# Optimization experiments

Measured on AMD Instinct MI355X. Metric: run time of the kernel, lower is better.

## Reference

```python
import jax, jax.numpy as jnp
import numpy as np

B, H, N, C, E, D, L_OUT, LAYERS = 16, 64, 512, 3, 128, 32, 12, 2


def setup_inputs() -> dict:
    key = jax.random.key(0)
    ks = jax.random.split(key, 16)
    nrm = lambda k, s, sc=1.0: jax.random.normal(k, s, jnp.float32) * sc
    adj = jax.random.uniform(ks[0], (N, N), jnp.float32)
    adj = adj / adj.sum(axis=-1, keepdims=True)  # row-normalized prior adjacency
    return {
        "x_input": nrm(ks[1], (B, H, N, C)),
        "adj": adj,
        "Wf": nrm(ks[2], (3, E, 3 * C), 0.1),
        "Uf": nrm(ks[3], (3, E, E), 0.05),
        "bf": jnp.zeros((3, E), jnp.float32),
        "E1f": nrm(ks[4], (N, D)),
        "E2f": nrm(ks[5], (N, D)),
        "Wb": nrm(ks[6], (3, E, 3 * C), 0.1),
        "Ub": nrm(ks[7], (3, E, E), 0.05),
        "bb": jnp.zeros((3, E), jnp.float32),
        "E1b": nrm(ks[8], (N, D)),
        "E2b": nrm(ks[9], (N, D)),
        "dec_w": nrm(ks[10], (L_OUT, LAYERS, 2 * E), 0.05),  # Conv2d(layer_num->out_len, k=(1,2E)) squeezed
        "dec_b": jnp.zeros((L_OUT,), jnp.float32),
        "out_w": nrm(ks[11], (L_OUT, L_OUT), 0.1),  # 1x1 Conv2d squeezed
        "out_b": jnp.zeros((L_OUT,), jnp.float32),
    }


def _cell_step(c, xt, adj, A_dyn, W, U, b):
    # Graph-coupled GRU cell (IBNCell): xt [B,C,N], c [B,E,N].
    msg = jnp.concatenate(
        [xt,
         jnp.einsum('bcn,nm->bcm', xt, adj),      # prior-graph message passing
         jnp.einsum('bcn,nm->bcm', xt, A_dyn)],   # learned dynamic-graph message passing
        axis=1)  # [B, 3C, N]
    gx = jnp.einsum('goc,bcn->gbon', W, msg)  # 3 stacked gate projections
    r = jax.nn.sigmoid(gx[0] + jnp.einsum('oe,ben->bon', U[0], c) + b[0][:, None])
    u = jax.nn.sigmoid(gx[1] + jnp.einsum('oe,ben->bon', U[1], c) + b[1][:, None])
    g = jnp.tanh(gx[2] + jnp.einsum('oe,ben->bon', U[2], r * c) + b[2][:, None])
    return u * c + (1.0 - u) * g


def _forward(x_input, adj, Wf, Uf, bf, E1f, E2f, Wb, Ub, bb, E1b, E2b, dec_w, dec_b, out_w, out_b):
    # torch: x_input.transpose(-3,-1).transpose(-2,-1) -> [B,C,H,N]; scan layout [H,B,C,N]
    xs = jnp.transpose(x_input, (1, 0, 3, 2))
    A_f = jax.nn.softmax(jax.nn.relu(E1f @ E2f.T), axis=-1)  # dynamic adjacency, fwd cell
    A_b = jax.nn.softmax(jax.nn.relu(E1b @ E2b.T), axis=-1)  # dynamic adjacency, back cell
    c0 = jnp.zeros((xs.shape[1], Wf.shape[1], xs.shape[3]), xs.dtype)  # [B,E,N]

    def step_f(c, xt):
        cn = _cell_step(c, xt, adj, A_f, Wf, Uf, bf)
        return cn, None

    # Output only depends on the last timestep of the bidirectional concat:
    # forward branch -> final state after H steps; backward branch (after flip)
    # at t=H-1 -> its FIRST step (input x[H-1]). Dead per-step outputs elided.
    h_fwd, _ = jax.lax.scan(step_f, c0, xs)
    h_back0 = _cell_step(c0, xs[-1], adj, A_b, Wb, Ub, bb)
    last_ht = jnp.concatenate([h_fwd, h_back0], axis=1)  # [B, 2E, N]

    lt = jnp.transpose(last_ht, (0, 2, 1))  # [B, N, 2E]
    # layer loop z>0 is a no-op on current_layer_output -> final_result repeats last_ht
    final = jnp.broadcast_to(lt[:, None], (lt.shape[0], LAYERS, lt.shape[1], lt.shape[2]))
    h = jnp.einsum('blne,ole->bon', final, dec_w) + dec_b[:, None]  # decoder conv (1,2E)
    return jnp.einsum('oi,bin->bon', out_w, h) + out_b[:, None]  # 1x1 output conv -> [B,L_OUT,N]


def reference(x_input, adj, Wf, Uf, bf, E1f, E2f, Wb, Ub, bb, E1b, E2b, dec_w, dec_b, out_w, out_b):
    return _forward(x_input, adj, Wf, Uf, bf, E1f, E2f, Wb, Ub, bb, E1b, E2b, dec_w, dec_b, out_w, out_b)
```

## Files before the change

kernel.cpp:

```cpp
#include <hip/hip_runtime.h>


typedef _Float16 half8_t __attribute__((ext_vector_type(8)));
typedef __fp16 fp16x2_t __attribute__((ext_vector_type(2)));
typedef float float4_t __attribute__((ext_vector_type(4)));

#define PIN(x) asm volatile("" : "+v"(x))

__device__ __forceinline__ float exp2_(float x) { return __builtin_amdgcn_exp2f(x); }
__device__ __forceinline__ float rcp_(float x) { return __builtin_amdgcn_rcpf(x); }

__global__ __launch_bounds__(256) void prep_kernel(
    const float* __restrict__ E1f, const float* __restrict__ E2f,
    const float* __restrict__ E1b, const float* __restrict__ E2b,
    const float* __restrict__ adj, const float* __restrict__ Wf,
    const float* __restrict__ Uf, const float* __restrict__ bf,
    const float* __restrict__ Wb, const float* __restrict__ bb,
    _Float16* __restrict__ adjT, _Float16* __restrict__ AfT,
    _Float16* __restrict__ AbT, _Float16* __restrict__ ufrag,
    _Float16* __restrict__ wbfrag, _Float16* __restrict__ zpad) {
  int bid = blockIdx.x;
  int tid = threadIdx.x;
  if (bid >= 1288) {
    if (tid < 64) zpad[tid] = (_Float16)0.f;
    return;
  }
  if (bid >= 1272) {
    int r2 = bid - 1272;
    int gi = 1 + (r2 & 1);
    int og = r2 >> 1;
    float scl = (gi == 2) ? 2.8853902f : -1.4426950f;
    for (int e = tid; e < 512; e += 256) {
      int lane = e >> 3, j = e & 7;
      int o = og * 16 + (lane & 15);
      int q = (lane >> 4) * 8 + j;
      float v = (q < 9) ? Wb[gi * 1152 + o * 9 + q]
                        : (q == 9 ? bb[gi * 128 + o] : 0.f);
      wbfrag[r2 * 512 + e] = (_Float16)(v * scl);
    }
    return;
  }
  if (bid >= 1152) {
    int r = bid - 1152;
    int kb = r % 5;
    int gi = (r / 5) % 3;
    int og = r / 15;
    float scl = (gi == 2) ? 2.8853902f : -1.4426950f;
    for (int e = tid; e < 512; e += 256) {
      int lane = e >> 3, j = e & 7;
      int o = og * 16 + (lane & 15);
      int q4 = lane >> 4;
      float v;
      if (kb < 4) {
        v = Uf[gi * 16384 + o * 128 + kb * 32 + q4 * 8 + j];
      } else {
        int q = q4 * 8 + j;
        v = (q < 9) ? Wf[gi * 1152 + o * 9 + q]
                    : (q == 9 ? bf[gi * 128 + o] : 0.f);
      }
      ufrag[r * 512 + e] = (_Float16)(v * scl);
    }
    return;
  }
  if (bid >= 1024) {
    int base = (bid - 1024) * 4;
    for (int r = 0; r < 4; ++r) {
      int row = base + r;
      float v0 = adj[row * 512 + tid];
      float v1 = adj[row * 512 + tid + 256];
      adjT[(size_t)tid * 512 + row] = (_Float16)v0;
      adjT[(size_t)(tid + 256) * 512 + row] = (_Float16)v1;
    }
    return;
  }
  int which = bid >> 9;
  int row = bid & 511;
  const float* E1 = which ? E1b : E1f;
  const float* E2 = which ? E2b : E2f;
  _Float16* A = which ? AbT : AfT;
  __shared__ float e1s[32];
  __shared__ float red[256];
  if (tid < 32) e1s[tid] = E1[row * 32 + tid];
  __syncthreads();
  float s[2];
#pragma unroll
  for (int h = 0; h < 2; ++h) {
    int m = tid + h * 256;
    const float4* e2 = (const float4*)(E2 + m * 32);
    float acc = 0.f;
#pragma unroll
    for (int d4 = 0; d4 < 8; ++d4) {
      float4 v = e2[d4];
      acc = fmaf(v.x, e1s[d4 * 4 + 0], acc);
      acc = fmaf(v.y, e1s[d4 * 4 + 1], acc);
      acc = fmaf(v.z, e1s[d4 * 4 + 2], acc);
      acc = fmaf(v.w, e1s[d4 * 4 + 3], acc);
    }
    s[h] = fmaxf(acc, 0.f);
  }
  red[tid] = fmaxf(s[0], s[1]);
  __syncthreads();
  for (int off = 128; off > 0; off >>= 1) {
    if (tid < off) red[tid] = fmaxf(red[tid], red[tid + off]);
    __syncthreads();
  }
  float mx = red[0];
  __syncthreads();
  float e0 = __expf(s[0] - mx), e1v = __expf(s[1] - mx);
  red[tid] = e0 + e1v;
  __syncthreads();
  for (int off = 128; off > 0; off >>= 1) {
    if (tid < off) red[tid] += red[tid + off];
    __syncthreads();
  }
  float inv = rcp_(red[0]);
  A[(size_t)tid * 512 + row] = (_Float16)(e0 * inv);
  A[(size_t)(tid + 256) * 512 + row] = (_Float16)(e1v * inv);
}

__global__ __launch_bounds__(256, 2) void msg_kernel(
    const float* __restrict__ x, const _Float16* __restrict__ adjT,
    const _Float16* __restrict__ AfT, const _Float16* __restrict__ AbT,
    _Float16* __restrict__ msg16, _Float16* __restrict__ msgb16) {
  __shared__ __align__(16) _Float16 Alds[48 * 512];
  __shared__ __align__(16) _Float16 Sst[1024 * 16];
  int tid = threadIdx.x;
  int t = blockIdx.x >> 3;
  int n0g = (blockIdx.x & 7) * 64;
  int lane = tid & 63, og = tid >> 6;
  int l15 = lane & 15, q4 = lane >> 4, q0 = q4 * 8;
  bool is63 = (t == 63);

  {
    int b = tid >> 4, li = tid & 15;
    const float4* xb = (const float4*)(x + (size_t)(b * 64 + t) * 1536);
#pragma unroll
    for (int k = 0; k < 24; ++k) {
      float4 v = xb[k * 16 + li];
      int j0 = (k * 16 + li) * 4;
#pragma unroll
      for (int e = 0; e < 4; ++e) {
        int j = j0 + e;
        int n = (j * 21846) >> 16;
        int c = j - n * 3;
        int m = b * 3 + c;
        float val = (e == 0) ? v.x : (e == 1) ? v.y : (e == 2) ? v.z : v.w;
        Alds[m * 512 + ((((n >> 3) ^ (m & 7)) << 3) | (n & 7))] = (_Float16)val;
      }
    }
  }
  __syncthreads();

  const float4_t zero4 = {0.f, 0.f, 0.f, 0.f};
  float4_t acc[3][2], accb[3];
#pragma unroll
  for (int mt = 0; mt < 3; ++mt) { acc[mt][0] = zero4; acc[mt][1] = zero4; accb[mt] = zero4; }

  int n = n0g + og * 16 + l15;
  for (int kb = 0; kb < 16; ++kb) {
    half8_t afr[3];
#pragma unroll
    for (int mt = 0; mt < 3; ++mt) {
      int m = mt * 16 + l15;
      afr[mt] = *(const half8_t*)&Alds[m * 512 + ((((kb * 4 + q4) ^ (m & 7)) << 3))];
    }
    half8_t b0 = *(const half8_t*)&adjT[(size_t)n * 512 + kb * 32 + q0];
    half8_t b1 = *(const half8_t*)&AfT[(size_t)n * 512 + kb * 32 + q0];
#pragma unroll
    for (int mt = 0; mt < 3; ++mt) {
      acc[mt][0] = __builtin_amdgcn_mfma_f32_16x16x32_f16(afr[mt], b0, acc[mt][0], 0, 0, 0);
      acc[mt][1] = __builtin_amdgcn_mfma_f32_16x16x32_f16(afr[mt], b1, acc[mt][1], 0, 0, 0);
    }
    if (is63) {
      half8_t b2 = *(const half8_t*)&AbT[(size_t)n * 512 + kb * 32 + q0];
#pragma unroll
      for (int mt = 0; mt < 3; ++mt)
        accb[mt] = __builtin_amdgcn_mfma_f32_16x16x32_f16(afr[mt], b2, accb[mt], 0, 0, 0);
    }
  }

  for (int i = tid; i < 1024; i += 256) {
    int tb = i >> 6, nl = i & 63;
    int nn = n0g + nl;
    _Float16* row = &Sst[i * 16];
#pragma unroll
    for (int c = 0; c < 3; ++c) {
      int m = tb * 3 + c;
      row[c] = Alds[m * 512 + ((((nn >> 3) ^ (m & 7)) << 3) | (nn & 7))];
    }
    row[9] = (_Float16)1.f;
#pragma unroll
    for (int z = 10; z < 16; ++z) row[z] = (_Float16)0.f;
  }
#pragma unroll
  for (int mt = 0; mt < 3; ++mt)
#pragma unroll
    for (int r = 0; r < 4; ++r) {
      int m = mt * 16 + q4 * 4 + r;
      int tb = (m * 21846) >> 16;
      int c = m - tb * 3;
      _Float16* row = &Sst[(tb * 64 + og * 16 + l15) * 16];
      row[3 + c] = (_Float16)acc[mt][0][r];
      row[6 + c] = (_Float16)acc[mt][1][r];
    }
  __syncthreads();
  for (int i = tid; i < 2048; i += 256) {
    int rrow = i >> 1, h = i & 1;
    int tb = rrow >> 6, nl = rrow & 63;
    ((uint4*)msg16)[(((size_t)(t * 16 + tb) * 512) + n0g + nl) * 2 + h] =
        ((const uint4*)Sst)[i];
  }
  if (is63) {
    __syncthreads();
#pragma unroll
    for (int mt = 0; mt < 3; ++mt)
#pragma unroll
      for (int r = 0; r < 4; ++r) {
        int m = mt * 16 + q4 * 4 + r;
        int tb = (m * 21846) >> 16;
        int c = m - tb * 3;
        Sst[(tb * 64 + og * 16 + l15) * 16 + 6 + c] = (_Float16)accb[mt][r];
      }
    __syncthreads();
    for (int i = tid; i < 2048; i += 256) {
      int rrow = i >> 1, h = i & 1;
      int tb = rrow >> 6, nl = rrow & 63;
      ((uint4*)msgb16)[(((size_t)tb * 512) + n0g + nl) * 2 + h] =
          ((const uint4*)Sst)[i];
    }
  }
}

__global__ __launch_bounds__(512, 4) void rec_kernel(
    const _Float16* __restrict__ msg16, const _Float16* __restrict__ msgb16,
    const _Float16* __restrict__ zpad, const _Float16* __restrict__ ufrag,
    const _Float16* __restrict__ wbfrag, const float* __restrict__ dec_w,
    const float* __restrict__ dec_b, const float* __restrict__ out_w,
    const float* __restrict__ out_b, float* __restrict__ out) {
  __shared__ __align__(16) _Float16 Cbuf[2048];
  __shared__ __align__(16) _Float16 Gbuf[2048];
  __shared__ float hf_lds[128 * 16];
  __shared__ float hb_lds[128 * 16];
  __shared__ float hdec_lds[12 * 16];
  int tid = threadIdx.x, bid = blockIdx.x;
  int b = bid >> 5;
  int nt = bid & 31;
  int n0 = nt * 16;
  int lane = tid & 63, og = tid >> 6;
  int l15 = lane & 15, q4 = lane >> 4;

  half8_t afrag[3][5];
#pragma unroll
  for (int gi = 0; gi < 3; ++gi)
#pragma unroll
    for (int kb = 0; kb < 5; ++kb) {
      afrag[gi][kb] = *(const half8_t*)
          &ufrag[(size_t)(((og * 3 + gi) * 5 + kb) * 512) + lane * 8];
      PIN(afrag[gi][kb]);
    }

  if (tid < 256) {
    uint4 z; z.x = z.y = z.z = z.w = 0;
    ((uint4*)Cbuf)[tid] = z;
  }
  float cr[4] = {0.f, 0.f, 0.f, 0.f};

  const float4_t zero4 = {0.f, 0.f, 0.f, 0.f};
  union H4U { fp16x2_t h2[2]; unsigned long long u; };
  const char* base = (const char*)msg16 +
                     ((size_t)(b * 512 + n0 + l15)) * 32 + (q4 & 1) * 16;
  const char* mrow = (q4 < 2) ? base : (const char*)zpad;
  size_t tstr = (q4 < 2) ? (size_t)16 * 512 * 32 : 0;
  half8_t bm = *(const half8_t*)mrow;

  int kb_w = og >> 1;
  int lane_w = ((og & 1) * 2 + (q4 >> 1)) * 16 + l15;
  int j0 = (q4 & 1) * 4;
  __syncthreads();

  for (int t = 0; t < 64; ++t) {
    int tn = (t < 63) ? t + 1 : 63;
    half8_t bm_n = *(const half8_t*)(mrow + (size_t)tn * tstr);

    half8_t cf[4];
#pragma unroll
    for (int kb = 0; kb < 4; ++kb)
      cf[kb] = *(const half8_t*)&Cbuf[(kb * 64 + lane) * 8];

    float4_t accr = zero4, accu = zero4;
#pragma unroll
    for (int kb = 0; kb < 4; ++kb) {
      accr = __builtin_amdgcn_mfma_f32_16x16x32_f16(afrag[0][kb], cf[kb], accr, 0, 0, 0);
      accu = __builtin_amdgcn_mfma_f32_16x16x32_f16(afrag[1][kb], cf[kb], accu, 0, 0, 0);
    }
    accr = __builtin_amdgcn_mfma_f32_16x16x32_f16(afrag[0][4], bm, accr, 0, 0, 0);
    accu = __builtin_amdgcn_mfma_f32_16x16x32_f16(afrag[1][4], bm, accu, 0, 0, 0);
    float4_t accg_p = __builtin_amdgcn_mfma_f32_16x16x32_f16(afrag[2][4], bm, zero4, 0, 0, 0);

    float uu[4];
    {
      H4U v;
#pragma unroll
      for (int r = 0; r < 2; ++r) {
        float a = rcp_(1.f + exp2_(accr[2 * r])) * cr[2 * r];
        float bq = rcp_(1.f + exp2_(accr[2 * r + 1])) * cr[2 * r + 1];
        v.h2[r] = __builtin_amdgcn_cvt_pkrtz(a, bq);
      }
      *(unsigned long long*)&Gbuf[(kb_w * 64 + lane_w) * 8 + j0] = v.u;
#pragma unroll
      for (int r = 0; r < 4; ++r) uu[r] = rcp_(1.f + exp2_(accu[r]));
    }
    __syncthreads();

    half8_t gf[4];
#pragma unroll
    for (int kb = 0; kb < 4; ++kb)
      gf[kb] = *(const half8_t*)&Gbuf[(kb * 64 + lane) * 8];
    float4_t accg = accg_p;
#pragma unroll
    for (int kb = 0; kb < 4; ++kb)
      accg = __builtin_amdgcn_mfma_f32_16x16x32_f16(afrag[2][kb], gf[kb], accg, 0, 0, 0);

    {
      H4U v;
      float cn[4];
#pragma unroll
      for (int r = 0; r < 4; ++r) {
        float gg = fmaf(-2.f, rcp_(exp2_(accg[r]) + 1.f), 1.f);
        cn[r] = fmaf(uu[r], cr[r] - gg, gg);
        cr[r] = cn[r];
      }
      v.h2[0] = __builtin_amdgcn_cvt_pkrtz(cn[0], cn[1]);
      v.h2[1] = __builtin_amdgcn_cvt_pkrtz(cn[2], cn[3]);
      *(unsigned long long*)&Cbuf[(kb_w * 64 + lane_w) * 8 + j0] = v.u;
    }
    __syncthreads();
    bm = bm_n;
  }

  {
    const char* bb_base = (const char*)msgb16 +
                          ((size_t)(b * 512 + n0 + l15)) * 32 + (q4 & 1) * 16;
    const char* bp = (q4 < 2) ? bb_base : (const char*)zpad;
    half8_t bbk = *(const half8_t*)bp;
    half8_t au_f = *(const half8_t*)&wbfrag[(size_t)((og * 2 + 0) * 512) + lane * 8];
    half8_t ag_f = *(const half8_t*)&wbfrag[(size_t)((og * 2 + 1) * 512) + lane * 8];
    float4_t au = __builtin_amdgcn_mfma_f32_16x16x32_f16(au_f, bbk, zero4, 0, 0, 0);
    float4_t ag = __builtin_amdgcn_mfma_f32_16x16x32_f16(ag_f, bbk, zero4, 0, 0, 0);
#pragma unroll
    for (int r = 0; r < 4; ++r) {
      int row = og * 16 + q4 * 4 + r;
      float uu2 = rcp_(1.f + exp2_(au[r]));
      float gg = fmaf(-2.f, rcp_(exp2_(ag[r]) + 1.f), 1.f);
      hb_lds[row * 16 + l15] = (1.f - uu2) * gg;
      hf_lds[row * 16 + l15] = cr[r];
    }
  }
  __syncthreads();

  if (tid < 192) {
    int i = tid >> 4, cc = tid & 15;
    const float* dwa = dec_w + (size_t)i * 512;
    const float* dwb = dwa + 256;
    float hd = dec_b[i];
    for (int e = 0; e < 128; ++e) {
      hd = fmaf(dwa[e] + dwb[e], hf_lds[e * 16 + cc], hd);
      hd = fmaf(dwa[128 + e] + dwb[128 + e], hb_lds[e * 16 + cc], hd);
    }
    hdec_lds[i * 16 + cc] = hd;
  }
  __syncthreads();
  if (tid < 192) {
    int o = tid >> 4, cc = tid & 15;
    float v = out_b[o];
#pragma unroll
    for (int i = 0; i < 12; ++i) v = fmaf(out_w[o * 12 + i], hdec_lds[i * 16 + cc], v);
    out[((size_t)(b * 12 + o)) * 512 + n0 + cc] = v;
  }
}

extern "C" void kernel_launch(void* const* d_in, const int* in_sizes, int n_in,
                              void* d_out, int out_size, void* d_ws, size_t ws_size,
                              hipStream_t stream) {
  (void)in_sizes; (void)n_in; (void)out_size; (void)ws_size;
  const float* x     = (const float*)d_in[0];
  const float* adj   = (const float*)d_in[1];
  const float* Wf    = (const float*)d_in[2];
  const float* Uf    = (const float*)d_in[3];
  const float* bf    = (const float*)d_in[4];
  const float* E1f   = (const float*)d_in[5];
  const float* E2f   = (const float*)d_in[6];
  const float* Wb    = (const float*)d_in[7];
  const float* bb    = (const float*)d_in[9];
  const float* E1b   = (const float*)d_in[10];
  const float* E2b   = (const float*)d_in[11];
  const float* dec_w = (const float*)d_in[12];
  const float* dec_b = (const float*)d_in[13];
  const float* out_w = (const float*)d_in[14];
  const float* out_b = (const float*)d_in[15];

  _Float16* h      = (_Float16*)d_ws;
  _Float16* adjT   = h;
  _Float16* AfT    = h + 262144;
  _Float16* AbT    = h + 524288;
  _Float16* ufrag  = h + 786432;
  _Float16* wbfrag = h + 847872;
  _Float16* zpad   = h + 856064;
  _Float16* msg16  = h + 856128;
  _Float16* msgb16 = h + 9244736;

  prep_kernel<<<1289, 256, 0, stream>>>(E1f, E2f, E1b, E2b, adj, Wf, Uf, bf,
                                        Wb, bb, adjT, AfT, AbT, ufrag, wbfrag, zpad);
  msg_kernel<<<512, 256, 0, stream>>>(x, adjT, AfT, AbT, msg16, msgb16);
  rec_kernel<<<512, 512, 0, stream>>>(msg16, msgb16, zpad, ufrag, wbfrag,
                                      dec_w, dec_b, out_w, out_b, (float*)d_out);
}
```

Baseline: 201.4 us.

## Pipeline next-step input MFMAs, raise MFMA priority, fuse GRU output reciprocals

The input-projection MFMAs for step t+1 now run at the end of step t, after the new state is written and before the barrier. This takes them off the serial dependency chain of the recurrence. The recurrent MFMA blocks are wrapped in s_setprio to favour them in scheduling. The update-gate sigmoid and the tanh candidate are merged algebraically into one fraction, so the state update needs a single reciprocal instead of two. The prefetch pointer now advances unconditionally, so the last iteration reads one timestep past the input, which may go out of bounds.

```diff
diff --git a/kernel.cpp b/kernel.cpp
--- a/kernel.cpp
+++ b/kernel.cpp
@@ -269,9 +269,13 @@
   union H4U { fp16x2_t h2[2]; unsigned long long u; };
   const char* base = (const char*)msg16 +
                      ((size_t)(b * 512 + n0 + l15)) * 32 + (q4 & 1) * 16;
-  const char* mrow = (q4 < 2) ? base : (const char*)zpad;
+  const char* pcur = (q4 < 2) ? base : (const char*)zpad;
   size_t tstr = (q4 < 2) ? (size_t)16 * 512 * 32 : 0;
-  half8_t bm = *(const half8_t*)mrow;
+
+  half8_t bm0 = *(const half8_t*)pcur;
+  float4_t accr_p = __builtin_amdgcn_mfma_f32_16x16x32_f16(afrag[0][4], bm0, zero4, 0, 0, 0);
+  float4_t accu_p = __builtin_amdgcn_mfma_f32_16x16x32_f16(afrag[1][4], bm0, zero4, 0, 0, 0);
+  float4_t accg_p = __builtin_amdgcn_mfma_f32_16x16x32_f16(afrag[2][4], bm0, zero4, 0, 0, 0);
 
   int kb_w = og >> 1;
   int lane_w = ((og & 1) * 2 + (q4 >> 1)) * 16 + l15;
@@ -279,25 +283,24 @@
   __syncthreads();
 
   for (int t = 0; t < 64; ++t) {
-    int tn = (t < 63) ? t + 1 : 63;
-    half8_t bm_n = *(const half8_t*)(mrow + (size_t)tn * tstr);
+    const char* pnext = pcur + tstr;
+    half8_t bm_n = *(const half8_t*)pnext;
 
     half8_t cf[4];
 #pragma unroll
     for (int kb = 0; kb < 4; ++kb)
       cf[kb] = *(const half8_t*)&Cbuf[(kb * 64 + lane) * 8];
 
-    float4_t accr = zero4, accu = zero4;
+    float4_t accr = accr_p, accu = accu_p;
+    __builtin_amdgcn_s_setprio(1);
 #pragma unroll
     for (int kb = 0; kb < 4; ++kb) {
       accr = __builtin_amdgcn_mfma_f32_16x16x32_f16(afrag[0][kb], cf[kb], accr, 0, 0, 0);
       accu = __builtin_amdgcn_mfma_f32_16x16x32_f16(afrag[1][kb], cf[kb], accu, 0, 0, 0);
     }
-    accr = __builtin_amdgcn_mfma_f32_16x16x32_f16(afrag[0][4], bm, accr, 0, 0, 0);
-    accu = __builtin_amdgcn_mfma_f32_16x16x32_f16(afrag[1][4], bm, accu, 0, 0, 0);
-    float4_t accg_p = __builtin_amdgcn_mfma_f32_16x16x32_f16(afrag[2][4], bm, zero4, 0, 0, 0);
-
-    float uu[4];
+    __builtin_amdgcn_s_setprio(0);
+
+    float Eu[4];
     {
       H4U v;
 #pragma unroll
@@ -308,7 +311,7 @@
       }
       *(unsigned long long*)&Gbuf[(kb_w * 64 + lane_w) * 8 + j0] = v.u;
 #pragma unroll
-      for (int r = 0; r < 4; ++r) uu[r] = rcp_(1.f + exp2_(accu[r]));
+      for (int r = 0; r < 4; ++r) Eu[r] = exp2_(accu[r]);
     }
     __syncthreads();
 
@@ -317,25 +320,33 @@
     for (int kb = 0; kb < 4; ++kb)
       gf[kb] = *(const half8_t*)&Gbuf[(kb * 64 + lane) * 8];
     float4_t accg = accg_p;
+    __builtin_amdgcn_s_setprio(1);
 #pragma unroll
     for (int kb = 0; kb < 4; ++kb)
       accg = __builtin_amdgcn_mfma_f32_16x16x32_f16(afrag[2][kb], gf[kb], accg, 0, 0, 0);
+    __builtin_amdgcn_s_setprio(0);
 
     {
       H4U v;
       float cn[4];
 #pragma unroll
       for (int r = 0; r < 4; ++r) {
-        float gg = fmaf(-2.f, rcp_(exp2_(accg[r]) + 1.f), 1.f);
-        cn[r] = fmaf(uu[r], cr[r] - gg, gg);
+        float Eg = exp2_(accg[r]);
+        float d0 = Eg + 1.f;
+        float den = fmaf(Eu[r], d0, d0);
+        float num = fmaf(cr[r], Eg, cr[r]) + fmaf(Eu[r], Eg, -Eu[r]);
+        cn[r] = num * rcp_(den);
         cr[r] = cn[r];
       }
       v.h2[0] = __builtin_amdgcn_cvt_pkrtz(cn[0], cn[1]);
       v.h2[1] = __builtin_amdgcn_cvt_pkrtz(cn[2], cn[3]);
       *(unsigned long long*)&Cbuf[(kb_w * 64 + lane_w) * 8 + j0] = v.u;
     }
-    __syncthreads();
-    bm = bm_n;
+    accr_p = __builtin_amdgcn_mfma_f32_16x16x32_f16(afrag[0][4], bm_n, zero4, 0, 0, 0);
+    accu_p = __builtin_amdgcn_mfma_f32_16x16x32_f16(afrag[1][4], bm_n, zero4, 0, 0, 0);
+    accg_p = __builtin_amdgcn_mfma_f32_16x16x32_f16(afrag[2][4], bm_n, zero4, 0, 0, 0);
+    __syncthreads();
+    pcur = pnext;
   }
 
   {
```

Result: no change. 198.4 us (-1.5%).
